# Kernel tuning notes

Hardware: AMD Instinct MI355X
Metric: run time of the kernel (lower is better)

Reference implementation:

```python
import jax, jax.numpy as jnp
import numpy as np

HC = 4
C = 256
TMAX = 20
RMS_EPS = 1e-6
PRE_EPS = 0.0
SINKHORN_EPS = 1e-6
POST_MULT = 2.0


def setup_inputs() -> dict:
    key = jax.random.key(0)
    k1, k2, k3 = jax.random.split(key, 3)
    B, S = 8, 4096
    m = HC * HC + 2 * HC
    x = jax.random.normal(k1, (B, S, HC, C), dtype=jnp.float32)
    phi = jax.random.normal(k2, (HC * C, m), dtype=jnp.float32) * 0.02
    b = jnp.zeros((m,), dtype=jnp.float32)
    W = jax.random.normal(k3, (C, C), dtype=jnp.float32) * (1.0 / np.sqrt(C))
    return {
        "x": x, "phi": phi, "b": b,
        "alpha_pre": jnp.float32(1.0), "alpha_post": jnp.float32(1.0), "alpha_res": jnp.float32(1.0),
        "W": W,
    }


def _mhc_coeffs(x, phi, b, alpha_pre, alpha_post, alpha_res):
    # x: [..., HC, C] -> flatten streams, project, RMS-normalize logits.
    lead = x.shape[:-2]
    v = x.reshape(lead + (HC * C,))
    logits = jnp.einsum('...k,km->...m', v, phi)            # [..., m]
    rms = jnp.sqrt(jnp.mean(logits * logits, axis=-1, keepdims=True) + RMS_EPS)
    y = logits / rms + b                                     # [..., m]
    pre = y[..., :HC]
    post = y[..., HC:2 * HC]
    res = y[..., 2 * HC:].reshape(lead + (HC, HC))
    h_pre = jax.nn.sigmoid(alpha_pre * pre) + PRE_EPS        # [..., HC]
    h_post = POST_MULT * jax.nn.sigmoid(alpha_post * post)   # [..., HC]
    # Sinkhorn-Knopp: make exp(alpha_res * res) approximately doubly stochastic.
    P = jnp.exp(alpha_res * res)                             # [..., HC, HC]

    def step(P, _):
        P = P / (jnp.sum(P, axis=-1, keepdims=True) + SINKHORN_EPS)  # row norm
        P = P / (jnp.sum(P, axis=-2, keepdims=True) + SINKHORN_EPS)  # col norm
        return P, None

    P, _ = jax.lax.scan(step, P, None, length=TMAX)
    return h_pre, h_post, P


def reference(x, phi, b, alpha_pre, alpha_post, alpha_res, W):
    h_pre, h_post, h_res = _mhc_coeffs(x, phi, b, alpha_pre, alpha_post, alpha_res)
    # Pre-aggregate streams: x_in = sum_i h_pre[i] * x[i]
    x_in = jnp.einsum('...i,...ic->...c', h_pre, x)          # [..., C]
    # Wrapped layer: nn.Linear(C, C, bias=False) -> x_in @ W.T
    f_out = x_in @ W.T                                       # [..., C]
    # Post + residual: x_out[o] = sum_i h_res[o,i]*x[i] + h_post[o]*f_out
    x_out = jnp.einsum('...oi,...ic->...oc', h_res, x) + h_post[..., :, None] * f_out[..., None, :]
    return x_out
```

## Files before the change

### kernel.cpp

```cpp
#include <hip/hip_runtime.h>

typedef __attribute__((ext_vector_type(4))) float floatx4;
typedef __attribute__((ext_vector_type(8))) short short8;

__device__ __forceinline__ unsigned short f2bf(float f) {
    union { float f; unsigned int i; } v; v.f = f;
    unsigned int x = v.i;
    unsigned int r = (x + 0x7FFFu + ((x >> 16) & 1u)) >> 16;
    return (unsigned short)r;
}
__device__ __forceinline__ float bf2f(unsigned short u) {
    union { unsigned int i; float f; } v; v.i = ((unsigned int)u) << 16;
    return v.f;
}

__global__ void mhc_prep(const float* __restrict__ phi, const float* __restrict__ W,
                         unsigned short* __restrict__ phiF, unsigned short* __restrict__ WF) {
    int e = blockIdx.x * 256 + threadIdx.x;
    if (e < 32768) {
        int j = e & 7, lane = (e >> 3) & 63, nt = (e >> 9) & 1, ks = e >> 10;
        int n = nt * 16 + (lane & 15);
        int k = ks * 32 + ((lane >> 4) & 3) * 8 + j;
        float v = (n < 24) ? phi[k * 24 + n] : 0.0f;
        phiF[e] = f2bf(v);
    } else {
        int e2 = e - 32768;
        int j = e2 & 7, lane = (e2 >> 3) & 63, ks = (e2 >> 9) & 7, nt = e2 >> 12;
        int n = nt * 16 + (lane & 15);
        int k = ks * 32 + ((lane >> 4) & 3) * 8 + j;
        WF[e2] = f2bf(W[n * 256 + k]);
    }
}

#define XS_STRIDE 1032
#define XIN_STRIDE 264
#define CO_STRIDE 28

__global__ __launch_bounds__(256) void mhc_main(
    const float* __restrict__ x, const float* __restrict__ bias,
    const float* __restrict__ s_ap, const float* __restrict__ s_apo,
    const float* __restrict__ s_ar,
    const unsigned short* __restrict__ phiF, const unsigned short* __restrict__ WF,
    float* __restrict__ out)
{
    __shared__ unsigned short xs[16 * XS_STRIDE];
    __shared__ unsigned short xin[16 * XIN_STRIDE];
    __shared__ float lg[16 * CO_STRIDE];
    __shared__ float coef[16 * CO_STRIDE];

    const int t = threadIdx.x;
    const int lane = t & 63;
    const int w = t >> 6;
    const int quad = lane >> 4;
    const int col = lane & 15;
    const long base = (long)blockIdx.x * (16 * 1024);

    {
        const float4* xg = (const float4*)(x + base);
        #pragma unroll
        for (int ii = 0; ii < 16; ++ii) {
            int lin = ii * 256 + t;
            float4 v = xg[lin];
            int tok = lin >> 8;
            int k = (lin & 255) * 4;
            uint2 pk;
            pk.x = (unsigned int)f2bf(v.x) | ((unsigned int)f2bf(v.y) << 16);
            pk.y = (unsigned int)f2bf(v.z) | ((unsigned int)f2bf(v.w) << 16);
            *reinterpret_cast<uint2*>(&xs[tok * XS_STRIDE + k]) = pk;
        }
    }
    __syncthreads();

    if (w < 2) {
        floatx4 acc = {0.0f, 0.0f, 0.0f, 0.0f};
        for (int ks = 0; ks < 32; ++ks) {
            short8 a = *reinterpret_cast<const short8*>(&xs[col * XS_STRIDE + ks * 32 + quad * 8]);
            short8 b = *reinterpret_cast<const short8*>(&phiF[(ks * 2 + w) * 512 + lane * 8]);
            acc = __builtin_amdgcn_mfma_f32_16x16x32_bf16(a, b, acc, 0, 0, 0);
        }
        int n = w * 16 + col;
        if (n < 24) {
            #pragma unroll
            for (int r = 0; r < 4; ++r)
                lg[(quad * 4 + r) * CO_STRIDE + n] = acc[r];
        }
    }
    __syncthreads();

    {
        int g = t >> 4, p = t & 15;
        float a = lg[g * CO_STRIDE + p];
        float b2 = (p < 8) ? lg[g * CO_STRIDE + 16 + p] : 0.0f;
        float s = a * a + b2 * b2;
        s += __shfl_xor(s, 1); s += __shfl_xor(s, 2);
        s += __shfl_xor(s, 4); s += __shfl_xor(s, 8);
        float rinv = 1.0f / sqrtf(s * (1.0f / 24.0f) + 1e-6f);
        float yP = lg[g * CO_STRIDE + 8 + p] * rinv + bias[8 + p];
        float P = expf(s_ar[0] * yP);
        for (int it = 0; it < 20; ++it) {
            float r = P + __shfl_xor(P, 1); r += __shfl_xor(r, 2);
            P *= __builtin_amdgcn_rcpf(r + 1e-6f);
            float c = P + __shfl_xor(P, 4); c += __shfl_xor(c, 8);
            P *= __builtin_amdgcn_rcpf(c + 1e-6f);
        }
        coef[g * CO_STRIDE + 8 + p] = P;
        if (p < 8) {
            float yh = a * rinv + bias[p];
            float h = (p < 4) ? 1.0f / (1.0f + expf(-s_ap[0] * yh))
                              : 2.0f / (1.0f + expf(-s_apo[0] * yh));
            coef[g * CO_STRIDE + p] = h;
        }
    }
    __syncthreads();

    {
        int c = t;
        #pragma unroll 4
        for (int tok = 0; tok < 16; ++tok) {
            float4 h4 = *reinterpret_cast<const float4*>(&coef[tok * CO_STRIDE]);
            const unsigned short* xr = &xs[tok * XS_STRIDE + c];
            float s = h4.x * bf2f(xr[0]) + h4.y * bf2f(xr[256])
                    + h4.z * bf2f(xr[512]) + h4.w * bf2f(xr[768]);
            xin[tok * XIN_STRIDE + c] = f2bf(s);
        }
    }
    __syncthreads();

    short8 afr[8];
    #pragma unroll
    for (int ks = 0; ks < 8; ++ks)
        afr[ks] = *reinterpret_cast<const short8*>(&xin[col * XIN_STRIDE + ks * 32 + quad * 8]);
    floatx4 accs[4];
    #pragma unroll
    for (int nt = 0; nt < 4; ++nt) {
        floatx4 acc = {0.0f, 0.0f, 0.0f, 0.0f};
        int ntile = w * 4 + nt;
        #pragma unroll
        for (int ks = 0; ks < 8; ++ks) {
            short8 b = *reinterpret_cast<const short8*>(&WF[(ntile * 8 + ks) * 512 + lane * 8]);
            acc = __builtin_amdgcn_mfma_f32_16x16x32_bf16(afr[ks], b, acc, 0, 0, 0);
        }
        accs[nt] = acc;
    }

    #pragma unroll
    for (int r = 0; r < 4; ++r) {
        int tok = quad * 4 + r;
        const float* cb = &coef[tok * CO_STRIDE];
        float4 hpo = *reinterpret_cast<const float4*>(cb + 4);
        float4 P0  = *reinterpret_cast<const float4*>(cb + 8);
        float4 P1  = *reinterpret_cast<const float4*>(cb + 12);
        float4 P2  = *reinterpret_cast<const float4*>(cb + 16);
        float4 P3  = *reinterpret_cast<const float4*>(cb + 20);
        long ob = base + (long)tok * 1024;
        #pragma unroll
        for (int nt = 0; nt < 4; ++nt) {
            int c = (w * 4 + nt) * 16 + col;
            float f = accs[nt][r];
            const unsigned short* xr = &xs[tok * XS_STRIDE + c];
            float x0 = bf2f(xr[0]),   x1 = bf2f(xr[256]);
            float x2 = bf2f(xr[512]), x3 = bf2f(xr[768]);
            out[ob + c]       = P0.x * x0 + P0.y * x1 + P0.z * x2 + P0.w * x3 + hpo.x * f;
            out[ob + 256 + c] = P1.x * x0 + P1.y * x1 + P1.z * x2 + P1.w * x3 + hpo.y * f;
            out[ob + 512 + c] = P2.x * x0 + P2.y * x1 + P2.z * x2 + P2.w * x3 + hpo.z * f;
            out[ob + 768 + c] = P3.x * x0 + P3.y * x1 + P3.z * x2 + P3.w * x3 + hpo.w * f;
        }
    }
}

extern "C" void kernel_launch(void* const* d_in, const int* in_sizes, int n_in,
                              void* d_out, int out_size, void* d_ws, size_t ws_size,
                              hipStream_t stream) {
    const float* x    = (const float*)d_in[0];
    const float* phi  = (const float*)d_in[1];
    const float* bias = (const float*)d_in[2];
    const float* ap   = (const float*)d_in[3];
    const float* apo  = (const float*)d_in[4];
    const float* ar   = (const float*)d_in[5];
    const float* W    = (const float*)d_in[6];
    float* out = (float*)d_out;

    unsigned short* phiF = (unsigned short*)d_ws;
    unsigned short* WF   = (unsigned short*)d_ws + 32768;

    mhc_prep<<<384, 256, 0, stream>>>(phi, W, phiF, WF);
    mhc_main<<<2048, 256, 0, stream>>>(x, bias, ap, apo, ar, phiF, WF, out);
}
```

Measured before the change: 262.6 us.

## Make main kernel persistent with register prefetch of next tile

Turns the main kernel into a persistent grid of 768 blocks that loop over tiles. Each block prefetches the next tile's x into registers while it computes the current one, so global loads overlap the MFMA and coefficient work. Adds packed bf16 conversion via v_cvt_pk_bf16_f32 and replaces the shuffles in the reductions and Sinkhorn loop with DPP moves. The 16 float4 prefetch registers increase register pressure under launch_bounds(256,3), and 2048 tiles over 768 blocks leaves the last round unevenly loaded.

```diff
diff --git a/kernel.cpp b/kernel.cpp
--- a/kernel.cpp
+++ b/kernel.cpp
@@ -12,6 +12,18 @@
 __device__ __forceinline__ float bf2f(unsigned short u) {
     union { unsigned int i; float f; } v; v.i = ((unsigned int)u) << 16;
     return v.f;
+}
+
+__device__ __forceinline__ unsigned int cvtpk_bf16(float lo, float hi) {
+    unsigned int r;
+    asm("v_cvt_pk_bf16_f32 %0, %1, %2" : "=v"(r) : "v"(lo), "v"(hi));
+    return r;
+}
+
+template<int CTRL>
+__device__ __forceinline__ float dppf(float x) {
+    return __int_as_float(__builtin_amdgcn_update_dpp(
+        0, __float_as_int(x), CTRL, 0xF, 0xF, false));
 }
 
 __global__ void mhc_prep(const float* __restrict__ phi, const float* __restrict__ W,
@@ -35,8 +47,9 @@
 #define XS_STRIDE 1032
 #define XIN_STRIDE 264
 #define CO_STRIDE 28
-
-__global__ __launch_bounds__(256) void mhc_main(
+#define NTILES 2048
+
+__global__ __launch_bounds__(256, 3) void mhc_main(
     const float* __restrict__ x, const float* __restrict__ bias,
     const float* __restrict__ s_ap, const float* __restrict__ s_apo,
     const float* __restrict__ s_ar,
@@ -53,118 +66,136 @@
     const int w = t >> 6;
     const int quad = lane >> 4;
     const int col = lane & 15;
-    const long base = (long)blockIdx.x * (16 * 1024);
-
+
+    int tile = blockIdx.x;
+    float4 pre[16];
     {
-        const float4* xg = (const float4*)(x + base);
+        const float4* xg = (const float4*)(x) + (long)tile * 4096;
+        #pragma unroll
+        for (int ii = 0; ii < 16; ++ii) pre[ii] = xg[ii * 256 + t];
+    }
+
+    for (;;) {
         #pragma unroll
         for (int ii = 0; ii < 16; ++ii) {
-            int lin = ii * 256 + t;
-            float4 v = xg[lin];
-            int tok = lin >> 8;
-            int k = (lin & 255) * 4;
             uint2 pk;
-            pk.x = (unsigned int)f2bf(v.x) | ((unsigned int)f2bf(v.y) << 16);
-            pk.y = (unsigned int)f2bf(v.z) | ((unsigned int)f2bf(v.w) << 16);
-            *reinterpret_cast<uint2*>(&xs[tok * XS_STRIDE + k]) = pk;
-        }
-    }
-    __syncthreads();
-
-    if (w < 2) {
-        floatx4 acc = {0.0f, 0.0f, 0.0f, 0.0f};
-        for (int ks = 0; ks < 32; ++ks) {
-            short8 a = *reinterpret_cast<const short8*>(&xs[col * XS_STRIDE + ks * 32 + quad * 8]);
-            short8 b = *reinterpret_cast<const short8*>(&phiF[(ks * 2 + w) * 512 + lane * 8]);
-            acc = __builtin_amdgcn_mfma_f32_16x16x32_bf16(a, b, acc, 0, 0, 0);
-        }
-        int n = w * 16 + col;
-        if (n < 24) {
+            pk.x = cvtpk_bf16(pre[ii].x, pre[ii].y);
+            pk.y = cvtpk_bf16(pre[ii].z, pre[ii].w);
+            *reinterpret_cast<uint2*>(&xs[ii * XS_STRIDE + t * 4]) = pk;
+        }
+        const int next = tile + (int)gridDim.x;
+        const bool has_next = (next < NTILES);
+        if (has_next) {
+            const float4* xg = (const float4*)(x) + (long)next * 4096;
             #pragma unroll
-            for (int r = 0; r < 4; ++r)
-                lg[(quad * 4 + r) * CO_STRIDE + n] = acc[r];
-        }
-    }
-    __syncthreads();
-
-    {
-        int g = t >> 4, p = t & 15;
-        float a = lg[g * CO_STRIDE + p];
-        float b2 = (p < 8) ? lg[g * CO_STRIDE + 16 + p] : 0.0f;
-        float s = a * a + b2 * b2;
-        s += __shfl_xor(s, 1); s += __shfl_xor(s, 2);
-        s += __shfl_xor(s, 4); s += __shfl_xor(s, 8);
-        float rinv = 1.0f / sqrtf(s * (1.0f / 24.0f) + 1e-6f);
-        float yP = lg[g * CO_STRIDE + 8 + p] * rinv + bias[8 + p];
-        float P = expf(s_ar[0] * yP);
-        for (int it = 0; it < 20; ++it) {
-            float r = P + __shfl_xor(P, 1); r += __shfl_xor(r, 2);
-            P *= __builtin_amdgcn_rcpf(r + 1e-6f);
-            float c = P + __shfl_xor(P, 4); c += __shfl_xor(c, 8);
-            P *= __builtin_amdgcn_rcpf(c + 1e-6f);
-        }
-        coef[g * CO_STRIDE + 8 + p] = P;
-        if (p < 8) {
-            float yh = a * rinv + bias[p];
-            float h = (p < 4) ? 1.0f / (1.0f + expf(-s_ap[0] * yh))
-                              : 2.0f / (1.0f + expf(-s_apo[0] * yh));
-            coef[g * CO_STRIDE + p] = h;
-        }
-    }
-    __syncthreads();
-
-    {
-        int c = t;
-        #pragma unroll 4
-        for (int tok = 0; tok < 16; ++tok) {
-            float4 h4 = *reinterpret_cast<const float4*>(&coef[tok * CO_STRIDE]);
-            const unsigned short* xr = &xs[tok * XS_STRIDE + c];
-            float s = h4.x * bf2f(xr[0]) + h4.y * bf2f(xr[256])
-                    + h4.z * bf2f(xr[512]) + h4.w * bf2f(xr[768]);
-            xin[tok * XIN_STRIDE + c] = f2bf(s);
-        }
-    }
-    __syncthreads();
-
-    short8 afr[8];
-    #pragma unroll
-    for (int ks = 0; ks < 8; ++ks)
-        afr[ks] = *reinterpret_cast<const short8*>(&xin[col * XIN_STRIDE + ks * 32 + quad * 8]);
-    floatx4 accs[4];
-    #pragma unroll
-    for (int nt = 0; nt < 4; ++nt) {
-        floatx4 acc = {0.0f, 0.0f, 0.0f, 0.0f};
-        int ntile = w * 4 + nt;
-        #pragma unroll
-        for (int ks = 0; ks < 8; ++ks) {
-            short8 b = *reinterpret_cast<const short8*>(&WF[(ntile * 8 + ks) * 512 + lane * 8]);
-            acc = __builtin_amdgcn_mfma_f32_16x16x32_bf16(afr[ks], b, acc, 0, 0, 0);
-        }
-        accs[nt] = acc;
-    }
-
-    #pragma unroll
-    for (int r = 0; r < 4; ++r) {
-        int tok = quad * 4 + r;
-        const float* cb = &coef[tok * CO_STRIDE];
-        float4 hpo = *reinterpret_cast<const float4*>(cb + 4);
-        float4 P0  = *reinterpret_cast<const float4*>(cb + 8);
-        float4 P1  = *reinterpret_cast<const float4*>(cb + 12);
-        float4 P2  = *reinterpret_cast<const float4*>(cb + 16);
-        float4 P3  = *reinterpret_cast<const float4*>(cb + 20);
-        long ob = base + (long)tok * 1024;
+            for (int ii = 0; ii < 16; ++ii) pre[ii] = xg[ii * 256 + t];
+        }
+        __syncthreads();
+
+        if (w < 2) {
+            floatx4 acc = {0.0f, 0.0f, 0.0f, 0.0f};
+            for (int ks = 0; ks < 32; ++ks) {
+                short8 a = *reinterpret_cast<const short8*>(&xs[col * XS_STRIDE + ks * 32 + quad * 8]);
+                short8 b = *reinterpret_cast<const short8*>(&phiF[(ks * 2 + w) * 512 + lane * 8]);
+                acc = __builtin_amdgcn_mfma_f32_16x16x32_bf16(a, b, acc, 0, 0, 0);
+            }
+            int n = w * 16 + col;
+            if (n < 24) {
+                #pragma unroll
+                for (int r = 0; r < 4; ++r)
+                    lg[(quad * 4 + r) * CO_STRIDE + n] = acc[r];
+            }
+        }
+        __syncthreads();
+
+        {
+            int g = t >> 4, p = t & 15;
+            float a = lg[g * CO_STRIDE + p];
+            float b2 = (p < 8) ? lg[g * CO_STRIDE + 16 + p] : 0.0f;
+            float s = a * a + b2 * b2;
+            s += dppf<0x121>(s);
+            s += dppf<0x122>(s);
+            s += dppf<0x124>(s);
+            s += dppf<0x128>(s);
+            float rinv = 1.0f / sqrtf(s * (1.0f / 24.0f) + 1e-6f);
+            float yP = lg[g * CO_STRIDE + 8 + p] * rinv + bias[8 + p];
+            float P = expf(s_ar[0] * yP);
+            for (int it = 0; it < 20; ++it) {
+                float r = P + dppf<0x39>(P);
+                r += dppf<0x4E>(r);
+                P *= __builtin_amdgcn_rcpf(r + 1e-6f);
+                float c = P + dppf<0x124>(P);
+                c += dppf<0x128>(c);
+                P *= __builtin_amdgcn_rcpf(c + 1e-6f);
+            }
+            coef[g * CO_STRIDE + 8 + p] = P;
+            if (p < 8) {
+                float yh = a * rinv + bias[p];
+                float h = (p < 4) ? 1.0f / (1.0f + expf(-s_ap[0] * yh))
+                                  : 2.0f / (1.0f + expf(-s_apo[0] * yh));
+                coef[g * CO_STRIDE + p] = h;
+            }
+        }
+        __syncthreads();
+
+        {
+            int c = t;
+            #pragma unroll 4
+            for (int tok = 0; tok < 16; ++tok) {
+                float4 h4 = *reinterpret_cast<const float4*>(&coef[tok * CO_STRIDE]);
+                const unsigned short* xr = &xs[tok * XS_STRIDE + c];
+                float s = h4.x * bf2f(xr[0]) + h4.y * bf2f(xr[256])
+                        + h4.z * bf2f(xr[512]) + h4.w * bf2f(xr[768]);
+                xin[tok * XIN_STRIDE + c] = f2bf(s);
+            }
+        }
+        __syncthreads();
+
+        short8 afr[8];
+        #pragma unroll
+        for (int ks = 0; ks < 8; ++ks)
+            afr[ks] = *reinterpret_cast<const short8*>(&xin[col * XIN_STRIDE + ks * 32 + quad * 8]);
+        floatx4 accs[4];
         #pragma unroll
         for (int nt = 0; nt < 4; ++nt) {
-            int c = (w * 4 + nt) * 16 + col;
-            float f = accs[nt][r];
-            const unsigned short* xr = &xs[tok * XS_STRIDE + c];
-            float x0 = bf2f(xr[0]),   x1 = bf2f(xr[256]);
-            float x2 = bf2f(xr[512]), x3 = bf2f(xr[768]);
-            out[ob + c]       = P0.x * x0 + P0.y * x1 + P0.z * x2 + P0.w * x3 + hpo.x * f;
-            out[ob + 256 + c] = P1.x * x0 + P1.y * x1 + P1.z * x2 + P1.w * x3 + hpo.y * f;
-            out[ob + 512 + c] = P2.x * x0 + P2.y * x1 + P2.z * x2 + P2.w * x3 + hpo.z * f;
-            out[ob + 768 + c] = P3.x * x0 + P3.y * x1 + P3.z * x2 + P3.w * x3 + hpo.w * f;
-        }
+            floatx4 acc = {0.0f, 0.0f, 0.0f, 0.0f};
+            int ntile = w * 4 + nt;
+            #pragma unroll
+            for (int ks = 0; ks < 8; ++ks) {
+                short8 b = *reinterpret_cast<const short8*>(&WF[(ntile * 8 + ks) * 512 + lane * 8]);
+                acc = __builtin_amdgcn_mfma_f32_16x16x32_bf16(afr[ks], b, acc, 0, 0, 0);
+            }
+            accs[nt] = acc;
+        }
+
+        const long base = (long)tile * 16384;
+        #pragma unroll
+        for (int r = 0; r < 4; ++r) {
+            int tok = quad * 4 + r;
+            const float* cb = &coef[tok * CO_STRIDE];
+            float4 hpo = *reinterpret_cast<const float4*>(cb + 4);
+            float4 P0  = *reinterpret_cast<const float4*>(cb + 8);
+            float4 P1  = *reinterpret_cast<const float4*>(cb + 12);
+            float4 P2  = *reinterpret_cast<const float4*>(cb + 16);
+            float4 P3  = *reinterpret_cast<const float4*>(cb + 20);
+            long ob = base + (long)tok * 1024;
+            #pragma unroll
+            for (int nt = 0; nt < 4; ++nt) {
+                int c = (w * 4 + nt) * 16 + col;
+                float f = accs[nt][r];
+                const unsigned short* xr = &xs[tok * XS_STRIDE + c];
+                float x0 = bf2f(xr[0]),   x1 = bf2f(xr[256]);
+                float x2 = bf2f(xr[512]), x3 = bf2f(xr[768]);
+                out[ob + c]       = P0.x * x0 + P0.y * x1 + P0.z * x2 + P0.w * x3 + hpo.x * f;
+                out[ob + 256 + c] = P1.x * x0 + P1.y * x1 + P1.z * x2 + P1.w * x3 + hpo.y * f;
+                out[ob + 512 + c] = P2.x * x0 + P2.y * x1 + P2.z * x2 + P2.w * x3 + hpo.z * f;
+                out[ob + 768 + c] = P3.x * x0 + P3.y * x1 + P3.z * x2 + P3.w * x3 + hpo.w * f;
+            }
+        }
+
+        tile = next;
+        if (!has_next) break;
+        __syncthreads();
     }
 }
 
@@ -184,5 +215,5 @@
     unsigned short* WF   = (unsigned short*)d_ws + 32768;
 
     mhc_prep<<<384, 256, 0, stream>>>(phi, W, phiF, WF);
-    mhc_main<<<2048, 256, 0, stream>>>(x, bias, ap, apo, ar, phiF, WF, out);
-}
+    mhc_main<<<768, 256, 0, stream>>>(x, bias, ap, apo, ar, phiF, WF, out);
+}
```

Result: slower. 329.1 us (+25.3%).

## Split fused kernel into coefficient and apply kernels, use DPP and packed bf16 converts

Applied to the files above, without the earlier changes.

Splits the single fused kernel in two. The first computes the RMS-normalized logits, sigmoids and Sinkhorn matrix per token and writes them to a workspace buffer. The second re-reads x from global memory in fp32 to do the pre-aggregation, the W matmul and the residual mix. It also spreads the phi projection over all four waves with a split-K reduction, replaces shuffles with DPP moves, and uses hardware packed bf16 conversion. The aim is less LDS pressure and higher occupancy, and the residual path now uses fp32 x instead of bf16. The cost is reading x twice from HBM (about 128MB each pass) plus an extra launch.

```diff
diff --git a/kernel.cpp b/kernel.cpp
--- a/kernel.cpp
+++ b/kernel.cpp
@@ -12,6 +12,18 @@
 __device__ __forceinline__ float bf2f(unsigned short u) {
     union { unsigned int i; float f; } v; v.i = ((unsigned int)u) << 16;
     return v.f;
+}
+
+__device__ __forceinline__ unsigned int cvtpk_bf16(float lo, float hi) {
+    unsigned int r;
+    asm("v_cvt_pk_bf16_f32 %0, %1, %2" : "=v"(r) : "v"(lo), "v"(hi));
+    return r;
+}
+
+template<int CTRL>
+__device__ __forceinline__ float dppf(float x) {
+    return __int_as_float(__builtin_amdgcn_update_dpp(
+        0, __float_as_int(x), CTRL, 0xF, 0xF, false));
 }
 
 __global__ void mhc_prep(const float* __restrict__ phi, const float* __restrict__ W,
@@ -33,20 +45,17 @@
 }
 
 #define XS_STRIDE 1032
-#define XIN_STRIDE 264
 #define CO_STRIDE 28
 
-__global__ __launch_bounds__(256) void mhc_main(
+__global__ __launch_bounds__(256) void mhc_coef(
     const float* __restrict__ x, const float* __restrict__ bias,
     const float* __restrict__ s_ap, const float* __restrict__ s_apo,
     const float* __restrict__ s_ar,
-    const unsigned short* __restrict__ phiF, const unsigned short* __restrict__ WF,
-    float* __restrict__ out)
+    const unsigned short* __restrict__ phiF,
+    float* __restrict__ cbuf)
 {
     __shared__ unsigned short xs[16 * XS_STRIDE];
-    __shared__ unsigned short xin[16 * XIN_STRIDE];
-    __shared__ float lg[16 * CO_STRIDE];
-    __shared__ float coef[16 * CO_STRIDE];
+    __shared__ float lgp[2][16 * CO_STRIDE];
 
     const int t = threadIdx.x;
     const int lane = t & 63;
@@ -64,64 +73,94 @@
             int tok = lin >> 8;
             int k = (lin & 255) * 4;
             uint2 pk;
-            pk.x = (unsigned int)f2bf(v.x) | ((unsigned int)f2bf(v.y) << 16);
-            pk.y = (unsigned int)f2bf(v.z) | ((unsigned int)f2bf(v.w) << 16);
+            pk.x = cvtpk_bf16(v.x, v.y);
+            pk.y = cvtpk_bf16(v.z, v.w);
             *reinterpret_cast<uint2*>(&xs[tok * XS_STRIDE + k]) = pk;
         }
     }
     __syncthreads();
 
-    if (w < 2) {
+    {
         floatx4 acc = {0.0f, 0.0f, 0.0f, 0.0f};
-        for (int ks = 0; ks < 32; ++ks) {
+        const int ntile = w & 1;
+        const int kh = w >> 1;
+        for (int ks = kh * 16; ks < kh * 16 + 16; ++ks) {
             short8 a = *reinterpret_cast<const short8*>(&xs[col * XS_STRIDE + ks * 32 + quad * 8]);
-            short8 b = *reinterpret_cast<const short8*>(&phiF[(ks * 2 + w) * 512 + lane * 8]);
+            short8 b = *reinterpret_cast<const short8*>(&phiF[(ks * 2 + ntile) * 512 + lane * 8]);
             acc = __builtin_amdgcn_mfma_f32_16x16x32_bf16(a, b, acc, 0, 0, 0);
         }
-        int n = w * 16 + col;
+        int n = ntile * 16 + col;
         if (n < 24) {
             #pragma unroll
             for (int r = 0; r < 4; ++r)
-                lg[(quad * 4 + r) * CO_STRIDE + n] = acc[r];
+                lgp[kh][(quad * 4 + r) * CO_STRIDE + n] = acc[r];
         }
     }
     __syncthreads();
 
     {
         int g = t >> 4, p = t & 15;
-        float a = lg[g * CO_STRIDE + p];
-        float b2 = (p < 8) ? lg[g * CO_STRIDE + 16 + p] : 0.0f;
+        float a  = lgp[0][g * CO_STRIDE + p]      + lgp[1][g * CO_STRIDE + p];
+        float b2 = (p < 8) ? (lgp[0][g * CO_STRIDE + 16 + p] + lgp[1][g * CO_STRIDE + 16 + p]) : 0.0f;
         float s = a * a + b2 * b2;
-        s += __shfl_xor(s, 1); s += __shfl_xor(s, 2);
-        s += __shfl_xor(s, 4); s += __shfl_xor(s, 8);
+        s += dppf<0x121>(s);
+        s += dppf<0x122>(s);
+        s += dppf<0x124>(s);
+        s += dppf<0x128>(s);
         float rinv = 1.0f / sqrtf(s * (1.0f / 24.0f) + 1e-6f);
-        float yP = lg[g * CO_STRIDE + 8 + p] * rinv + bias[8 + p];
+        float lr = lgp[0][g * CO_STRIDE + 8 + p] + lgp[1][g * CO_STRIDE + 8 + p];
+        float yP = lr * rinv + bias[8 + p];
         float P = expf(s_ar[0] * yP);
         for (int it = 0; it < 20; ++it) {
-            float r = P + __shfl_xor(P, 1); r += __shfl_xor(r, 2);
+            float r = P + dppf<0x39>(P);
+            r += dppf<0x4E>(r);
             P *= __builtin_amdgcn_rcpf(r + 1e-6f);
-            float c = P + __shfl_xor(P, 4); c += __shfl_xor(c, 8);
+            float c = P + dppf<0x124>(P);
+            c += dppf<0x128>(c);
             P *= __builtin_amdgcn_rcpf(c + 1e-6f);
         }
-        coef[g * CO_STRIDE + 8 + p] = P;
+        long tok = (long)blockIdx.x * 16 + g;
+        cbuf[tok * 24 + 8 + p] = P;
         if (p < 8) {
             float yh = a * rinv + bias[p];
             float h = (p < 4) ? 1.0f / (1.0f + expf(-s_ap[0] * yh))
                               : 2.0f / (1.0f + expf(-s_apo[0] * yh));
-            coef[g * CO_STRIDE + p] = h;
-        }
-    }
-    __syncthreads();
-
-    {
-        int c = t;
+            cbuf[tok * 24 + p] = h;
+        }
+    }
+}
+
+#define XIN_STRIDE 264
+
+__global__ __launch_bounds__(256) void mhc_apply(
+    const float* __restrict__ x, const float* __restrict__ cbuf,
+    const unsigned short* __restrict__ WF, float* __restrict__ out)
+{
+    __shared__ unsigned short xin[16 * XIN_STRIDE];
+    __shared__ float coef[16 * 24];
+
+    const int t = threadIdx.x;
+    const int lane = t & 63;
+    const int w = t >> 6;
+    const int quad = lane >> 4;
+    const int col = lane & 15;
+    const long base = (long)blockIdx.x * (16 * 1024);
+
+    {
+        const float* cg = cbuf + (long)blockIdx.x * 384;
+        coef[t] = cg[t];
+        if (t < 128) coef[256 + t] = cg[256 + t];
+    }
+    __syncthreads();
+
+    {
+        const float* xb = x + base + t;
         #pragma unroll 4
         for (int tok = 0; tok < 16; ++tok) {
-            float4 h4 = *reinterpret_cast<const float4*>(&coef[tok * CO_STRIDE]);
-            const unsigned short* xr = &xs[tok * XS_STRIDE + c];
-            float s = h4.x * bf2f(xr[0]) + h4.y * bf2f(xr[256])
-                    + h4.z * bf2f(xr[512]) + h4.w * bf2f(xr[768]);
-            xin[tok * XIN_STRIDE + c] = f2bf(s);
+            float4 h4 = *reinterpret_cast<const float4*>(&coef[tok * 24]);
+            const float* xr = xb + tok * 1024;
+            float s = h4.x * xr[0] + h4.y * xr[256] + h4.z * xr[512] + h4.w * xr[768];
+            xin[tok * XIN_STRIDE + t] = f2bf(s);
         }
     }
     __syncthreads();
@@ -146,20 +185,20 @@
     #pragma unroll
     for (int r = 0; r < 4; ++r) {
         int tok = quad * 4 + r;
-        const float* cb = &coef[tok * CO_STRIDE];
+        const float* cb = &coef[tok * 24];
         float4 hpo = *reinterpret_cast<const float4*>(cb + 4);
         float4 P0  = *reinterpret_cast<const float4*>(cb + 8);
         float4 P1  = *reinterpret_cast<const float4*>(cb + 12);
         float4 P2  = *reinterpret_cast<const float4*>(cb + 16);
         float4 P3  = *reinterpret_cast<const float4*>(cb + 20);
         long ob = base + (long)tok * 1024;
+        const float* xr0 = x + ob;
         #pragma unroll
         for (int nt = 0; nt < 4; ++nt) {
             int c = (w * 4 + nt) * 16 + col;
             float f = accs[nt][r];
-            const unsigned short* xr = &xs[tok * XS_STRIDE + c];
-            float x0 = bf2f(xr[0]),   x1 = bf2f(xr[256]);
-            float x2 = bf2f(xr[512]), x3 = bf2f(xr[768]);
+            float x0 = xr0[c],       x1 = xr0[256 + c];
+            float x2 = xr0[512 + c], x3 = xr0[768 + c];
             out[ob + c]       = P0.x * x0 + P0.y * x1 + P0.z * x2 + P0.w * x3 + hpo.x * f;
             out[ob + 256 + c] = P1.x * x0 + P1.y * x1 + P1.z * x2 + P1.w * x3 + hpo.y * f;
             out[ob + 512 + c] = P2.x * x0 + P2.y * x1 + P2.z * x2 + P2.w * x3 + hpo.z * f;
@@ -182,7 +221,9 @@
 
     unsigned short* phiF = (unsigned short*)d_ws;
     unsigned short* WF   = (unsigned short*)d_ws + 32768;
+    float* cbuf = (float*)((char*)d_ws + 196608);
 
     mhc_prep<<<384, 256, 0, stream>>>(phi, W, phiF, WF);
-    mhc_main<<<2048, 256, 0, stream>>>(x, bias, ap, apo, ar, phiF, WF, out);
-}
+    mhc_coef<<<2048, 256, 0, stream>>>(x, bias, ap, apo, ar, phiF, cbuf);
+    mhc_apply<<<2048, 256, 0, stream>>>(x, cbuf, WF, out);
+}
```

Result: slower. 284.2 us (+8.2%).
